# Optimization experiments

Measured on AMD Instinct MI355X. Metric: run time of the kernel, lower is better.

Reference implementation:

```python
import jax, jax.numpy as jnp
import numpy as np

B, TE, TD, EH, DH = 128, 512, 128, 512, 512
K_CNN, C_CNN = 7, 105

def setup_inputs() -> dict:
    key = jax.random.key(0)
    ks = jax.random.split(key, 20)
    n = lambda k, shp: jax.random.normal(k, shp, dtype=jnp.float32) * 0.05
    return {
        "LSTM": jax.random.normal(ks[0], (B, TE, EH), dtype=jnp.float32),
        "CNNs": jax.random.normal(ks[1], (B, K_CNN, C_CNN), dtype=jnp.float32),
        "Wa_w": n(ks[2], (TD, DH)), "Wa_b": n(ks[3], (TD,)),
        "Ua_w": n(ks[4], (TE, EH)), "Ua_b": n(ks[5], (TE,)),
        "va_w": n(ks[6], (1, TE + TD)), "va_b": n(ks[7], (1,)),
        "phi_w": n(ks[8], (EH, TE)), "phi_b": n(ks[9], (EH,)),
        "Wih": n(ks[10], (4 * DH, C_CNN + EH)), "Whh": n(ks[11], (4 * DH, DH)),
        "bih": n(ks[12], (4 * DH,)), "bhh": n(ks[13], (4 * DH,)),
        "wij_w": n(ks[14], (K_CNN, DH + C_CNN)), "wij_b": n(ks[15], (K_CNN,)),
        "s_i": jax.random.uniform(ks[16], (B, DH), dtype=jnp.float32),
        "m_i": jax.random.uniform(ks[17], (B, DH), dtype=jnp.float32),
    }

def reference(LSTM, CNNs, Wa_w, Wa_b, Ua_w, Ua_b, va_w, va_b, phi_w, phi_b,
              Wih, Whh, bih, bhh, wij_w, wij_b, s_i, m_i):
    Bn, Te, Eh = LSTM.shape
    Td = Wa_w.shape[0]
    Dh = s_i.shape[1]
    # delta_i_j for all j: strict lower-triangular one-hots [Te, Te]
    Dm = jnp.tril(jnp.ones((Te, Te), LSTM.dtype), k=-1)
    phi = Dm @ phi_w.T + phi_b                     # [Te, Eh]
    ph = phi[None, :, :] * LSTM                    # [B, Te, Eh] phi_delta * LSTM[:, j]
    Ua = jnp.einsum('bte,se->bts', ph, Ua_w) + Ua_b  # [B, Te, Te]
    Wa = s_i @ Wa_w.T + Wa_b                       # [B, Td] (same for all i, j)
    cat = jnp.concatenate([jnp.broadcast_to(Wa[:, None, :], (Bn, Te, Td)), Ua], axis=-1)
    Cw = jnp.tanh(cat) * va_w[0]                   # [B, Te, Td+Te]
    # one-hot mask picks index i + Te - j; v_a reduces to a single gathered term + bias
    idx = jnp.arange(Td)[:, None] + Te - jnp.arange(Te)[None, :]   # [Td, Te]
    e = Cw[:, jnp.arange(Te)[None, :], idx] + va_b[0]              # [B, Td, Te]
    a = jax.nn.softmax(e, axis=-1)
    c_i = jnp.einsum('bit,bte->bie', a, LSTM)      # [B, Td, Eh]
    # CNN attention (same for all decoder steps; note non-standard normalizer kept faithfully)
    w_cnn, w_s = wij_w[:, :C_CNN], wij_w[:, C_CNN:]
    ep = jnp.tanh(jnp.einsum('bkc,kc->bk', CNNs, w_cnn) + s_i @ w_s.T + wij_b)  # [B, K]
    ap = jnp.exp(ep) / jnp.sum(ep)
    c_p = jnp.einsum('bk,bkc->bc', ap, CNNs)       # [B, C_CNN]
    # LSTMCell with fixed (s_i, m_i) state => all decoder steps vectorize over i
    x = jnp.concatenate([c_i, jnp.broadcast_to(c_p[:, None, :], (Bn, Td, C_CNN))], axis=-1)
    gates = jnp.einsum('bid,gd->big', x, Wih) + bih + (s_i @ Whh.T + bhh)[:, None, :]
    ig, fg, gg, og = jnp.split(gates, 4, axis=-1)
    cnew = jax.nn.sigmoid(fg) * m_i[:, None, :] + jax.nn.sigmoid(ig) * jnp.tanh(gg)
    h = jax.nn.sigmoid(og) * jnp.tanh(cnew)        # [B, Td, Dh]
    return h
```

## Files before the change

kernel.cpp:

```cpp
#include <hip/hip_runtime.h>
#include <hip/hip_bf16.h>

#define B_   128
#define TE_  512
#define TD_  128
#define EH_  512
#define DH_  512
#define KC_  7
#define CC_  105
#define G_   2048
#define KX_  617
#define KP_  640
#define GNT  10

typedef __attribute__((ext_vector_type(8))) short bf16x8;
typedef __attribute__((ext_vector_type(4))) float f32x4;

__device__ __forceinline__ float sigm(float x){ return 1.f/(1.f + __expf(-x)); }
__device__ __forceinline__ float tanhf_fast(float x){
  float e = __expf(2.f*x);
  return 1.f - 2.f/(e + 1.f);
}

__device__ __forceinline__ unsigned short f2bf(float f){
  unsigned int u = __float_as_uint(f);
  unsigned int r = (u + 0x7fffu + ((u >> 16) & 1u)) >> 16;
  return (unsigned short)r;
}

typedef __attribute__((address_space(3))) unsigned int lds_u32_t;
typedef __attribute__((address_space(1))) const unsigned int glb_u32_t;
__device__ __forceinline__ void gload16(const void* g, void* l) {
  __builtin_amdgcn_global_load_lds((glb_u32_t*)g, (lds_u32_t*)l, 16, 0, 0);
}

static const size_t OFF_PHI  = 0;
static const size_t OFF_WA   = OFF_PHI  + (size_t)TE_*EH_*4;
static const size_t OFF_HPRE = OFF_WA   + (size_t)B_*TD_*4;
static const size_t OFF_EP   = OFF_HPRE + (size_t)B_*G_*4;
static const size_t OFF_CP   = OFF_EP   + 4096;
static const size_t OFF_ET   = ((OFF_CP + (size_t)B_*CC_*4 + 255)/256)*256;
static const size_t OFF_STAT = OFF_ET + (size_t)B_*TE_*TD_*4;
static const size_t OFF_P    = ((OFF_STAT + (size_t)2*B_*TD_*4 + 255)/256)*256;
static const size_t OFF_LT   = OFF_P  + (size_t)B_*TD_*TE_*2;
static const size_t OFF_WR   = OFF_LT + (size_t)B_*TE_*EH_*2;
static const size_t OFF_PT   = OFF_P;
static const size_t OFF_SUM  = OFF_PT + (size_t)TE_*EH_*4;
static const size_t OFF_WT   = OFF_P + (size_t)2*1024*1024;
static const size_t OFF_WAT  = OFF_P + (size_t)6*1024*1024;

__global__ __launch_bounds__(256) void k_tr(const float* __restrict__ src,
                                            float* __restrict__ dst, int R, int C) {
  int r0 = blockIdx.x * 64, c0 = blockIdx.y * 64;
  __shared__ float tile[64][65];
  int tid = threadIdx.x;
  int r = tid >> 2, c16 = (tid & 3) * 16;
  const float4* s4 = (const float4*)(src + (size_t)(r0 + r)*C + c0 + c16);
  float4 v0 = s4[0], v1 = s4[1], v2 = s4[2], v3 = s4[3];
  *(float4*)&tile[r][c16]    = v0;
  *(float4*)&tile[r][c16+4]  = v1;
  *(float4*)&tile[r][c16+8]  = v2;
  *(float4*)&tile[r][c16+12] = v3;
  __syncthreads();
  float o[16];
  #pragma unroll
  for (int j = 0; j < 16; ++j) o[j] = tile[c16+j][r];
  float* d = dst + (size_t)(c0 + r)*R + r0 + c16;
  *(float4*)d      = *(float4*)&o[0];
  *(float4*)(d+4)  = *(float4*)&o[4];
  *(float4*)(d+8)  = *(float4*)&o[8];
  *(float4*)(d+12) = *(float4*)&o[12];
}

__global__ void k_phiA(const float* __restrict__ phiT, float* __restrict__ phi,
                       float* __restrict__ sums) {
  int e = blockIdx.x * 256 + threadIdx.x;
  int z = blockIdx.y;
  float acc = 0.f;
  for (int t = z*64; t < z*64 + 64; ++t) {
    phi[(size_t)t*EH_ + e] = acc;
    acc += phiT[(size_t)t*EH_ + e];
  }
  sums[z*EH_ + e] = acc;
}
__global__ void k_phiB(const float* __restrict__ sums, const float* __restrict__ phi_b,
                       float* __restrict__ phi) {
  int e = blockIdx.x * 256 + threadIdx.x;
  int z = blockIdx.y;
  float off = phi_b[e];
  for (int zz = 0; zz < z; ++zz) off += sums[zz*EH_ + e];
  for (int t = z*64; t < z*64 + 64; ++t)
    phi[(size_t)t*EH_ + e] += off;
}

__global__ __launch_bounds__(256) void k_wa2(const float* __restrict__ s_i,
                                             const float* __restrict__ WaT,
                                             const float* __restrict__ Wa_b,
                                             const float* __restrict__ va_w,
                                             float* __restrict__ wa) {
  int lane = threadIdx.x & 63, wv = threadIdx.x >> 6;
  int b = blockIdx.x * 4 + wv;
  int d0 = lane * 2;
  const float2* w = (const float2*)WaT + lane;
  const float* s = s_i + (size_t)b*DH_;
  float ax = 0.f, ay = 0.f;
  #pragma unroll 8
  for (int k = 0; k < DH_; ++k) {
    float2 wv2 = w[(size_t)k*64];
    float x = s[k];
    ax += wv2.x * x; ay += wv2.y * x;
  }
  wa[b*TD_ + d0]     = tanhf_fast(ax + Wa_b[d0])     * va_w[d0];
  wa[b*TD_ + d0 + 1] = tanhf_fast(ay + Wa_b[d0 + 1]) * va_w[d0 + 1];
}

__global__ __launch_bounds__(64) void k_hpre2(const float* __restrict__ s_i,
                                              const float* __restrict__ WhhT,
                                              const float* __restrict__ bih,
                                              const float* __restrict__ bhh,
                                              float* __restrict__ hpre) {
  int gq = blockIdx.x * 64 + threadIdx.x;
  int b0 = blockIdx.y * 2;
  const float4* w = (const float4*)WhhT + gq;
  const float* s0 = s_i + (size_t)b0*DH_;
  const float* s1 = s0 + DH_;
  float4 a0 = {0.f,0.f,0.f,0.f}, a1 = {0.f,0.f,0.f,0.f};
  #pragma unroll 8
  for (int k = 0; k < DH_; ++k) {
    float4 wv = w[(size_t)k*512];
    float x0 = s0[k], x1 = s1[k];
    a0.x += wv.x*x0; a0.y += wv.y*x0; a0.z += wv.z*x0; a0.w += wv.w*x0;
    a1.x += wv.x*x1; a1.y += wv.y*x1; a1.z += wv.z*x1; a1.w += wv.w*x1;
  }
  int g = gq * 4;
  float4 bi = *(const float4*)(bih + g);
  float4 bh = *(const float4*)(bhh + g);
  float4 o0, o1;
  o0.x = a0.x + bi.x + bh.x; o0.y = a0.y + bi.y + bh.y;
  o0.z = a0.z + bi.z + bh.z; o0.w = a0.w + bi.w + bh.w;
  o1.x = a1.x + bi.x + bh.x; o1.y = a1.y + bi.y + bh.y;
  o1.z = a1.z + bi.z + bh.z; o1.w = a1.w + bi.w + bh.w;
  *(float4*)(hpre + (size_t)b0*G_ + g)       = o0;
  *(float4*)(hpre + (size_t)(b0+1)*G_ + g)   = o1;
}

__global__ __launch_bounds__(256) void k_ep(const float* __restrict__ CNNs,
                                            const float* __restrict__ wij_w,
                                            const float* __restrict__ wij_b,
                                            const float* __restrict__ s_i,
                                            float* __restrict__ ep) {
  int gw = blockIdx.x * 4 + (threadIdx.x >> 6);
  int lane = threadIdx.x & 63;
  if (gw >= B_*KC_) return;
  int b = gw / KC_, k = gw % KC_;
  const float* cr = CNNs + (size_t)(b*KC_ + k)*CC_;
  const float* wr = wij_w + (size_t)k*KX_;
  float acc = 0.f;
  for (int c = lane; c < CC_; c += 64) acc += cr[c] * wr[c];
  const float* sr = s_i + (size_t)b*DH_;
  const float* wsr = wr + CC_;
  #pragma unroll
  for (int j = 0; j < 8; ++j) { int h = lane + j*64; acc += sr[h] * wsr[h]; }
  #pragma unroll
  for (int m = 32; m; m >>= 1) acc += __shfl_xor(acc, m, 64);
  if (lane == 0) ep[gw] = tanhf_fast(acc + wij_b[k]);
}

__global__ void k_cnn_fin(const float* __restrict__ ep, const float* __restrict__ CNNs,
                          float* __restrict__ cp) {
  __shared__ float red[1024];
  __shared__ float apl[B_*KC_];
  int tid = threadIdx.x;
  red[tid] = (tid < B_*KC_) ? ep[tid] : 0.f;
  __syncthreads();
  for (int off = 512; off > 0; off >>= 1) {
    if (tid < off) red[tid] += red[tid + off];
    __syncthreads();
  }
  float S = red[0];
  if (tid < B_*KC_) apl[tid] = __expf(ep[tid]) / S;
  __syncthreads();
  for (int idx = tid; idx < B_*CC_; idx += blockDim.x) {
    int b = idx / CC_, c = idx % CC_;
    float acc = 0.f;
    #pragma unroll
    for (int k = 0; k < KC_; ++k)
      acc += apl[b*KC_ + k] * CNNs[(size_t)(b*KC_ + k)*CC_ + c];
    cp[idx] = acc;
  }
}

__global__ void k_cvtW(const float* __restrict__ Wih, unsigned short* __restrict__ Wr) {
  int id = blockIdx.x * 256 + threadIdx.x;
  int nr = id / 80, c8 = (id % 80) * 8;
  int gate = nr & 3, dh = nr >> 2;
  const float* src = Wih + (size_t)(gate*DH_ + dh)*KX_;
  unsigned short o[8];
  #pragma unroll
  for (int j = 0; j < 8; ++j) {
    int col = c8 + j;
    o[j] = (col < KX_) ? f2bf(src[col]) : 0;
  }
  *(uint4*)(Wr + (size_t)nr*KP_ + c8) = *(uint4*)o;
}

__global__ __launch_bounds__(256) void k_ltrans(const float* __restrict__ LSTM,
                                                unsigned short* __restrict__ LT) {
  int e0 = blockIdx.x * 64, t0 = blockIdx.y * 64, b = blockIdx.z;
  __shared__ float tile[64][65];
  int tid = threadIdx.x;
  int tt = tid >> 2, c16 = (tid & 3) * 16;
  const float4* src = (const float4*)(LSTM + ((size_t)b*TE_ + t0 + tt)*EH_ + e0 + c16);
  float4 v0 = src[0], v1 = src[1], v2 = src[2], v3 = src[3];
  *(float4*)&tile[tt][c16]    = v0;
  *(float4*)&tile[tt][c16+4]  = v1;
  *(float4*)&tile[tt][c16+8]  = v2;
  *(float4*)&tile[tt][c16+12] = v3;
  __syncthreads();
  int e = tid >> 2, t16 = (tid & 3) * 16;
  unsigned short o[16];
  #pragma unroll
  for (int j = 0; j < 16; ++j) o[j] = f2bf(tile[t16+j][e]);
  unsigned short* dst = LT + ((size_t)b*EH_ + e0 + e)*TE_ + t0 + t16;
  *(uint4*)dst     = *(uint4*)&o[0];
  *(uint4*)(dst+8) = *(uint4*)&o[8];
}

#define BMM_M 64
#define LDA_  40
#define LDB_  40
#define OTS_  132
__global__ __launch_bounds__(256) void k_bandmm(const float* __restrict__ LSTM,
                                                const float* __restrict__ phi,
                                                const float* __restrict__ Ua_w,
                                                const float* __restrict__ Ua_b,
                                                const float* __restrict__ va_w,
                                                const float* __restrict__ va_b,
                                                const float* __restrict__ wa,
                                                float* __restrict__ ET) {
  int t0 = blockIdx.x * BMM_M;
  int b  = blockIdx.y;
  int s_base = 321 - t0;
  __shared__ __align__(16) char smem[BMM_M * OTS_ * 4];
  short* sA = (short*)smem;
  short* sB = (short*)(smem + BMM_M*LDA_*2);
  int tid = threadIdx.x;
  int wave = tid >> 6, lane = tid & 63;
  int quad = lane >> 4, l16 = lane & 15;

  f32x4 acc[4][3];
  #pragma unroll
  for (int m = 0; m < 4; ++m)
    #pragma unroll
    for (int n = 0; n < 3; ++n)
      acc[m][n] = (f32x4){0.f, 0.f, 0.f, 0.f};

  int arow = tid >> 2;
  int ach  = (tid & 3) * 8;
  int aq   = ach >> 2;

  const float4* baseL = (const float4*)(LSTM + ((size_t)b*TE_ + t0 + arow)*EH_);
  const float4* baseP = (const float4*)(phi + (size_t)(t0 + arow)*EH_);
  const float4* baseU[3];
  int brow[3], bch[3];
  #pragma unroll
  for (int c = 0; c < 3; ++c) {
    int idx = c*256 + tid;
    brow[c] = idx >> 2;
    bch[c]  = (idx & 3) * 8;
    int s = s_base + brow[c];
    int sc = s < 0 ? 0 : (s > 511 ? 511 : s);
    baseU[c] = (const float4*)(Ua_w + (size_t)sc*EH_ + bch[c]);
  }

  float4 l0 = baseL[aq], l1 = baseL[aq+1], p0 = baseP[aq], p1 = baseP[aq+1];
  float4 u0[3], u1[3];
  #pragma unroll
  for (int c = 0; c < 3; ++c) { u0[c] = baseU[c][0]; u1[c] = baseU[c][1]; }

  for (int k0 = 0; k0 < EH_; k0 += 32) {
    unsigned short at[8];
    at[0]=f2bf(l0.x*p0.x); at[1]=f2bf(l0.y*p0.y); at[2]=f2bf(l0.z*p0.z); at[3]=f2bf(l0.w*p0.w);
    at[4]=f2bf(l1.x*p1.x); at[5]=f2bf(l1.y*p1.y); at[6]=f2bf(l1.z*p1.z); at[7]=f2bf(l1.w*p1.w);
    unsigned short bt[3][8];
    #pragma unroll
    for (int c = 0; c < 3; ++c) {
      bt[c][0]=f2bf(u0[c].x); bt[c][1]=f2bf(u0[c].y); bt[c][2]=f2bf(u0[c].z); bt[c][3]=f2bf(u0[c].w);
      bt[c][4]=f2bf(u1[c].x); bt[c][5]=f2bf(u1[c].y); bt[c][6]=f2bf(u1[c].z); bt[c][7]=f2bf(u1[c].w);
    }
    if (k0 + 32 < EH_) {
      int q = (k0 + 32) >> 2;
      l0 = baseL[q+aq]; l1 = baseL[q+aq+1]; p0 = baseP[q+aq]; p1 = baseP[q+aq+1];
      #pragma unroll
      for (int c = 0; c < 3; ++c) { u0[c] = baseU[c][q]; u1[c] = baseU[c][q+1]; }
    }
    __syncthreads();
    *(uint4*)&sA[arow*LDA_ + ach] = *(uint4*)at;
    #pragma unroll
    for (int c = 0; c < 3; ++c)
      *(uint4*)&sB[brow[c]*LDB_ + bch[c]] = *(uint4*)bt[c];
    __syncthreads();
    bf16x8 bfr[3];
    #pragma unroll
    for (int n = 0; n < 3; ++n)
      bfr[n] = *(const bf16x8*)&sB[(l16 + (wave*3 + n)*16)*LDB_ + quad*8];
    #pragma unroll
    for (int m = 0; m < 4; ++m) {
      bf16x8 af = *(const bf16x8*)&sA[(l16 + m*16)*LDA_ + quad*8];
      #pragma unroll
      for (int n = 0; n < 3; ++n)
        acc[m][n] = __builtin_amdgcn_mfma_f32_16x16x32_bf16(af, bfr[n], acc[m][n], 0, 0, 0);
    }
  }

  __syncthreads();
  float* tileO = (float*)smem;
  float vb = va_b[0];
  #pragma unroll
  for (int n = 0; n < 3; ++n) {
    int s = s_base + wave*48 + n*16 + l16;
    float ub = (s >= 0 && s < TE_) ? Ua_b[s] : 0.f;
    float vw = (s >= 0 && s < TE_) ? va_w[TD_ + s] : 0.f;
    #pragma unroll
    for (int m = 0; m < 4; ++m) {
      #pragma unroll
      for (int r = 0; r < 4; ++r) {
        int tl = m*16 + quad*4 + r;
        int i = s + t0 + tl - 384;
        if (i >= 0 && i < TD_) {
          float val;
          if (s >= 0) val = tanhf_fast(acc[m][n][r] + ub) * vw + vb;
          else        val = wa[b*TD_ + s + 128] + vb;
          tileO[tl*OTS_ + i] = val;
        }
      }
    }
  }
  __syncthreads();
  {
    int rsub = tid >> 5, c4 = (tid & 31) * 4;
    #pragma unroll
    for (int p = 0; p < 8; ++p) {
      int row = p*8 + rsub;
      float4 v = *(const float4*)&tileO[row*OTS_ + c4];
      *(float4*)(ET + ((size_t)b*TE_ + t0 + row)*TD_ + c4) = v;
    }
  }
}

__global__ __launch_bounds__(256) void k_stats(const float* __restrict__ ET,
                                               float* __restrict__ stat) {
  int i0 = blockIdx.x * 64, b = blockIdx.y;
  __shared__ float red[4][64], smax[64];
  int tid = threadIdx.x;
  int q = tid >> 6, il = tid & 63;
  const float* col = ET + (size_t)b*TE_*TD_ + i0 + il;
  float m = -1e30f;
  for (int t = q*128; t < q*128 + 128; ++t) m = fmaxf(m, col[(size_t)t*TD_]);
  red[q][il] = m;
  __syncthreads();
  if (tid < 64) {
    float mm = fmaxf(fmaxf(red[0][tid], red[1][tid]), fmaxf(red[2][tid], red[3][tid]));
    smax[tid] = mm;
  }
  __syncthreads();
  float mm = smax[il];
  float s = 0.f;
  for (int t = q*128; t < q*128 + 128; ++t) s += __expf(col[(size_t)t*TD_] - mm);
  __syncthreads();
  red[q][il] = s;
  __syncthreads();
  if (tid < 64) {
    float ss = red[0][tid] + red[1][tid] + red[2][tid] + red[3][tid];
    stat[b*TD_ + i0 + tid] = smax[tid];
    stat[(size_t)B_*TD_ + b*TD_ + i0 + tid] = 1.f/ss;
  }
}

__global__ __launch_bounds__(256) void k_trP(const float* __restrict__ ET,
                                             const float* __restrict__ stat,
                                             unsigned short* __restrict__ P) {
  int t0 = blockIdx.x * 64, i0 = blockIdx.y * 64, b = blockIdx.z;
  __shared__ float tile[64][65];
  __shared__ float smL[64], svL[64];
  int tid = threadIdx.x;
  if (tid < 64) {
    smL[tid] = stat[b*TD_ + i0 + tid];
    svL[tid] = stat[(size_t)B_*TD_ + b*TD_ + i0 + tid];
  }
  int tt = tid >> 2, c16 = (tid & 3) * 16;
  const float4* src = (const float4*)(ET + ((size_t)b*TE_ + t0 + tt)*TD_ + i0 + c16);
  float4 v[4]; v[0] = src[0]; v[1] = src[1]; v[2] = src[2]; v[3] = src[3];
  __syncthreads();
  const float* vf = (const float*)v;
  #pragma unroll
  for (int j = 0; j < 16; ++j)
    tile[tt][c16+j] = __expf(vf[j] - smL[c16+j]) * svL[c16+j];
  __syncthreads();
  int i = tid >> 2, t16 = (tid & 3) * 16;
  unsigned short o[16];
  #pragma unroll
  for (int j = 0; j < 16; ++j) o[j] = f2bf(tile[t16+j][i]);
  unsigned short* dst = P + ((size_t)b*TD_ + i0 + i)*TE_ + t0 + t16;
  *(uint4*)dst     = *(uint4*)&o[0];
  *(uint4*)(dst+8) = *(uint4*)&o[8];
}

__global__ void k_cp_fill(const float* __restrict__ cp, unsigned short* __restrict__ X) {
  int id = blockIdx.x * 256 + threadIdx.x;
  int m = id >> 4, c8 = (id & 15) * 8;
  int b = m >> 7;
  unsigned short o[8];
  #pragma unroll
  for (int j = 0; j < 8; ++j) {
    int c = c8 + j;
    o[j] = (c < CC_) ? f2bf(cp[b*CC_ + c]) : 0;
  }
  *(uint4*)(X + (size_t)m*KP_ + EH_ + c8) = *(uint4*)o;
}

#define CI_LD 40
__global__ __launch_bounds__(256) void k_ci_mm(const unsigned short* __restrict__ P,
                                               const unsigned short* __restrict__ LT,
                                               unsigned short* __restrict__ X) {
  int b = blockIdx.x, e0 = blockIdx.y * 128;
  __shared__ short sA[128 * CI_LD];
  __shared__ short sB[128 * CI_LD];
  int tid = threadIdx.x;
  int wave = tid >> 6, lane = tid & 63, quad = lane >> 4, l16 = lane & 15;
  int wm = wave >> 1, wn = wave & 1;
  int row = tid >> 1, ho = (tid & 1) * 16;

  const unsigned short* pa = P + ((size_t)b*TD_ + row)*TE_ + ho;
  const unsigned short* pb = LT + ((size_t)b*EH_ + e0 + row)*TE_ + ho;

  f32x4 acc[4][4];
  #pragma unroll
  for (int m = 0; m < 4; ++m)
    #pragma unroll
    for (int n = 0; n < 4; ++n)
      acc[m][n] = (f32x4){0.f, 0.f, 0.f, 0.f};

  uint4 a0 = *(const uint4*)pa, a1 = *(const uint4*)(pa + 8);
  uint4 b0 = *(const uint4*)pb, b1 = *(const uint4*)(pb + 8);

  for (int k0 = 0; k0 < TE_; k0 += 32) {
    uint4 na0, na1, nb0, nb1;
    if (k0 + 32 < TE_) {
      na0 = *(const uint4*)(pa + k0 + 32); na1 = *(const uint4*)(pa + k0 + 40);
      nb0 = *(const uint4*)(pb + k0 + 32); nb1 = *(const uint4*)(pb + k0 + 40);
    }
    __syncthreads();
    *(uint4*)&sA[row*CI_LD + ho]     = a0;
    *(uint4*)&sA[row*CI_LD + ho + 8] = a1;
    *(uint4*)&sB[row*CI_LD + ho]     = b0;
    *(uint4*)&sB[row*CI_LD + ho + 8] = b1;
    __syncthreads();
    bf16x8 bfr[4];
    #pragma unroll
    for (int n = 0; n < 4; ++n)
      bfr[n] = *(const bf16x8*)&sB[(wn*64 + n*16 + l16)*CI_LD + quad*8];
    #pragma unroll
    for (int m = 0; m < 4; ++m) {
      bf16x8 af = *(const bf16x8*)&sA[(wm*64 + m*16 + l16)*CI_LD + quad*8];
      #pragma unroll
      for (int n = 0; n < 4; ++n)
        acc[m][n] = __builtin_amdgcn_mfma_f32_16x16x32_bf16(af, bfr[n], acc[m][n], 0, 0, 0);
    }
    a0 = na0; a1 = na1; b0 = nb0; b1 = nb1;
  }

  #pragma unroll
  for (int m = 0; m < 4; ++m) {
    int i = wm*64 + m*16 + quad*4;
    #pragma unroll
    for (int n = 0; n < 4; ++n) {
      int e = e0 + wn*64 + n*16 + l16;
      unsigned short* xp = X + ((size_t)b*TD_ + i)*KP_ + e;
      #pragma unroll
      for (int r = 0; r < 4; ++r)
        xp[(size_t)r*KP_] = f2bf(acc[m][n][r]);
    }
  }
}

__global__ __launch_bounds__(512, 2) void k_gates8(const unsigned short* __restrict__ Wr,
                                                   const unsigned short* __restrict__ X,
                                                   const float* __restrict__ hpre,
                                                   const float* __restrict__ m_i,
                                                   float* __restrict__ out) {
  __shared__ short lds[4 * 256 * 64];
  const int g0  = blockIdx.x * 256;
  const int mi0 = blockIdx.y * 256;
  const int tid  = threadIdx.x;
  const int wave = tid >> 6, lane = tid & 63;
  const int l16 = lane & 15, quad = lane >> 4;
  const int wr = wave >> 2, wc = wave & 3;

  const int srow8 = lane >> 3;
  const int sch   = (lane & 7) ^ srow8;
  const unsigned short* gA = Wr + (size_t)(g0  + wave*8 + srow8) * KP_ + sch*8;
  const unsigned short* gB = X  + (size_t)(mi0 + wave*8 + srow8) * KP_ + sch*8;
  short* lA0 = lds;
  short* lB0 = lds + 16384;
  short* lA1 = lds + 32768;
  short* lB1 = lds + 49152;

  f32x4 acc[8][4];
  #pragma unroll
  for (int m = 0; m < 8; ++m)
    #pragma unroll
    for (int n = 0; n < 4; ++n) acc[m][n] = (f32x4){0.f, 0.f, 0.f, 0.f};

  auto stage = [&](int kt, int bf) {
    short* la = bf ? lA1 : lA0;
    short* lb = bf ? lB1 : lB0;
    const unsigned short* ga = gA + kt*64;
    const unsigned short* gb = gB + kt*64;
    #pragma unroll
    for (int r = 0; r < 4; ++r) {
      gload16(ga + (size_t)r*64*KP_, la + (r*8 + wave)*512);
      gload16(gb + (size_t)r*64*KP_, lb + (r*8 + wave)*512);
    }
  };

  stage(0, 0);
  __syncthreads();

  const int x7 = l16 & 7;
  for (int kt = 0; kt < GNT; ++kt) {
    const int cur = kt & 1;
    if (kt + 1 < GNT) stage(kt + 1, cur ^ 1);
    const short* la = cur ? lA1 : lA0;
    const short* lb = cur ? lB1 : lB0;
    #pragma unroll
    for (int ks = 0; ks < 2; ++ks) {
      const int ck = ((((ks << 2) | quad) ^ x7) << 3);
      bf16x8 bv[4];
      #pragma unroll
      for (int n = 0; n < 4; ++n)
        bv[n] = *(const bf16x8*)&lb[(wc*64 + n*16 + l16)*64 + ck];
      #pragma unroll
      for (int qm = 0; qm < 2; ++qm) {
        bf16x8 av[4];
        #pragma unroll
        for (int m = 0; m < 4; ++m)
          av[m] = *(const bf16x8*)&la[(wr*128 + qm*64 + m*16 + l16)*64 + ck];
        __builtin_amdgcn_s_setprio(1);
        #pragma unroll
        for (int m = 0; m < 4; ++m)
          #pragma unroll
          for (int n = 0; n < 4; ++n)
            acc[qm*4 + m][n] = __builtin_amdgcn_mfma_f32_16x16x32_bf16(av[m], bv[n], acc[qm*4 + m][n], 0, 0, 0);
        __builtin_amdgcn_s_setprio(0);
      }
    }
    __syncthreads();
  }

  const int bb = (mi0 >> 7) + (wc >> 1);
  const float* hp = hpre + (size_t)bb * G_;
  #pragma unroll
  for (int M = 0; M < 8; ++M) {
    const int dh = (g0 >> 2) + wr*32 + M*4 + quad;
    float h0 = hp[dh], h1 = hp[DH_ + dh], h2 = hp[2*DH_ + dh], h3 = hp[3*DH_ + dh];
    float miv = m_i[(size_t)bb*DH_ + dh];
    #pragma unroll
    for (int n = 0; n < 4; ++n) {
      int mi = mi0 + wc*64 + n*16 + l16;
      float ig = acc[M][n][0] + h0;
      float fg = acc[M][n][1] + h1;
      float gg = acc[M][n][2] + h2;
      float og = acc[M][n][3] + h3;
      float c  = sigm(fg)*miv + sigm(ig)*tanhf_fast(gg);
      float h  = sigm(og)*tanhf_fast(c);
      out[(size_t)mi*DH_ + dh] = h;
    }
  }
}

extern "C" void kernel_launch(void* const* d_in, const int* in_sizes, int n_in,
                              void* d_out, int out_size, void* d_ws, size_t ws_size,
                              hipStream_t stream) {
  (void)in_sizes; (void)n_in; (void)out_size; (void)ws_size;
  const float* LSTM  = (const float*)d_in[0];
  const float* CNNs  = (const float*)d_in[1];
  const float* Wa_w  = (const float*)d_in[2];
  const float* Wa_b  = (const float*)d_in[3];
  const float* Ua_w  = (const float*)d_in[4];
  const float* Ua_b  = (const float*)d_in[5];
  const float* va_w  = (const float*)d_in[6];
  const float* va_b  = (const float*)d_in[7];
  const float* phi_w = (const float*)d_in[8];
  const float* phi_b = (const float*)d_in[9];
  const float* Wih   = (const float*)d_in[10];
  const float* Whh   = (const float*)d_in[11];
  const float* bih   = (const float*)d_in[12];
  const float* bhh   = (const float*)d_in[13];
  const float* wij_w = (const float*)d_in[14];
  const float* wij_b = (const float*)d_in[15];
  const float* s_i   = (const float*)d_in[16];
  const float* m_i   = (const float*)d_in[17];
  float* out = (float*)d_out;
  char* ws = (char*)d_ws;

  float* phi  = (float*)(ws + OFF_PHI);
  float* wa   = (float*)(ws + OFF_WA);
  float* hpre = (float*)(ws + OFF_HPRE);
  float* ep   = (float*)(ws + OFF_EP);
  float* cp   = (float*)(ws + OFF_CP);
  float* stat = (float*)(ws + OFF_STAT);
  float* ET   = (float*)(ws + OFF_ET);
  unsigned short* X  = (unsigned short*)(ws + OFF_ET);
  unsigned short* P  = (unsigned short*)(ws + OFF_P);
  unsigned short* LT = (unsigned short*)(ws + OFF_LT);
  unsigned short* Wr = (unsigned short*)(ws + OFF_WR);
  float* phiT        = (float*)(ws + OFF_PT);
  float* sums        = (float*)(ws + OFF_SUM);
  float* WhhT        = (float*)(ws + OFF_WT);
  float* WaT         = (float*)(ws + OFF_WAT);

  k_tr      <<<dim3(8,8),      dim3(256),  0, stream>>>(phi_w, phiT, 512, 512);
  k_tr      <<<dim3(32,8),     dim3(256),  0, stream>>>(Whh, WhhT, 2048, 512);
  k_tr      <<<dim3(2,8),      dim3(256),  0, stream>>>(Wa_w, WaT, 128, 512);
  k_phiA    <<<dim3(2,8),      dim3(256),  0, stream>>>(phiT, phi, sums);
  k_phiB    <<<dim3(2,8),      dim3(256),  0, stream>>>(sums, phi_b, phi);
  k_wa2     <<<dim3(32),       dim3(256),  0, stream>>>(s_i, WaT, Wa_b, va_w, wa);
  k_hpre2   <<<dim3(8,64),     dim3(64),   0, stream>>>(s_i, WhhT, bih, bhh, hpre);
  k_ep      <<<dim3(224),      dim3(256),  0, stream>>>(CNNs, wij_w, wij_b, s_i, ep);
  k_cnn_fin <<<dim3(1),        dim3(1024), 0, stream>>>(ep, CNNs, cp);
  k_cvtW    <<<dim3(640),      dim3(256),  0, stream>>>(Wih, Wr);
  k_ltrans  <<<dim3(8,8,128),  dim3(256),  0, stream>>>(LSTM, LT);
  k_bandmm  <<<dim3(8,128),    dim3(256),  0, stream>>>(LSTM, phi, Ua_w, Ua_b, va_w, va_b, wa, ET);
  k_stats   <<<dim3(2,128),    dim3(256),  0, stream>>>(ET, stat);
  k_trP     <<<dim3(8,2,128),  dim3(256),  0, stream>>>(ET, stat, P);
  k_cp_fill <<<dim3(1024),     dim3(256),  0, stream>>>(cp, X);
  k_ci_mm   <<<dim3(128,4),    dim3(256),  0, stream>>>(P, LT, X);
  k_gates8  <<<dim3(8,64),     dim3(512),  0, stream>>>(Wr, X, hpre, m_i, out);
}
```

Before: 532.6 us.

## Fuse softmax stats and transpose into one LDS-tiled kernel; fuse CNN context fill

Measured after the change: 489.0 us. 8.2% less time.

```diff
diff --git a/kernel.cpp b/kernel.cpp
--- a/kernel.cpp
+++ b/kernel.cpp
@@ -114,34 +114,29 @@
   wa[b*TD_ + d0 + 1] = tanhf_fast(ay + Wa_b[d0 + 1]) * va_w[d0 + 1];
 }
 
-__global__ __launch_bounds__(64) void k_hpre2(const float* __restrict__ s_i,
-                                              const float* __restrict__ WhhT,
-                                              const float* __restrict__ bih,
-                                              const float* __restrict__ bhh,
-                                              float* __restrict__ hpre) {
-  int gq = blockIdx.x * 64 + threadIdx.x;
-  int b0 = blockIdx.y * 2;
+__global__ __launch_bounds__(256) void k_hpre2(const float* __restrict__ s_i,
+                                               const float* __restrict__ WhhT,
+                                               const float* __restrict__ bih,
+                                               const float* __restrict__ bhh,
+                                               float* __restrict__ hpre) {
+  int gq = blockIdx.x * 256 + threadIdx.x;
+  int b  = blockIdx.y;
   const float4* w = (const float4*)WhhT + gq;
-  const float* s0 = s_i + (size_t)b0*DH_;
-  const float* s1 = s0 + DH_;
-  float4 a0 = {0.f,0.f,0.f,0.f}, a1 = {0.f,0.f,0.f,0.f};
+  const float* s = s_i + (size_t)b*DH_;
+  float4 a = {0.f,0.f,0.f,0.f};
   #pragma unroll 8
   for (int k = 0; k < DH_; ++k) {
     float4 wv = w[(size_t)k*512];
-    float x0 = s0[k], x1 = s1[k];
-    a0.x += wv.x*x0; a0.y += wv.y*x0; a0.z += wv.z*x0; a0.w += wv.w*x0;
-    a1.x += wv.x*x1; a1.y += wv.y*x1; a1.z += wv.z*x1; a1.w += wv.w*x1;
+    float x = s[k];
+    a.x += wv.x*x; a.y += wv.y*x; a.z += wv.z*x; a.w += wv.w*x;
   }
   int g = gq * 4;
   float4 bi = *(const float4*)(bih + g);
   float4 bh = *(const float4*)(bhh + g);
-  float4 o0, o1;
-  o0.x = a0.x + bi.x + bh.x; o0.y = a0.y + bi.y + bh.y;
-  o0.z = a0.z + bi.z + bh.z; o0.w = a0.w + bi.w + bh.w;
-  o1.x = a1.x + bi.x + bh.x; o1.y = a1.y + bi.y + bh.y;
-  o1.z = a1.z + bi.z + bh.z; o1.w = a1.w + bi.w + bh.w;
-  *(float4*)(hpre + (size_t)b0*G_ + g)       = o0;
-  *(float4*)(hpre + (size_t)(b0+1)*G_ + g)   = o1;
+  float4 o;
+  o.x = a.x + bi.x + bh.x; o.y = a.y + bi.y + bh.y;
+  o.z = a.z + bi.z + bh.z; o.w = a.w + bi.w + bh.w;
+  *(float4*)(hpre + (size_t)b*G_ + g) = o;
 }
 
 __global__ __launch_bounds__(256) void k_ep(const float* __restrict__ CNNs,
@@ -166,10 +161,8 @@
   if (lane == 0) ep[gw] = tanhf_fast(acc + wij_b[k]);
 }
 
-__global__ void k_cnn_fin(const float* __restrict__ ep, const float* __restrict__ CNNs,
-                          float* __restrict__ cp) {
+__global__ void k_epsum(const float* __restrict__ ep, float* __restrict__ epsum) {
   __shared__ float red[1024];
-  __shared__ float apl[B_*KC_];
   int tid = threadIdx.x;
   red[tid] = (tid < B_*KC_) ? ep[tid] : 0.f;
   __syncthreads();
@@ -177,17 +170,28 @@
     if (tid < off) red[tid] += red[tid + off];
     __syncthreads();
   }
-  float S = red[0];
-  if (tid < B_*KC_) apl[tid] = __expf(ep[tid]) / S;
-  __syncthreads();
-  for (int idx = tid; idx < B_*CC_; idx += blockDim.x) {
-    int b = idx / CC_, c = idx % CC_;
-    float acc = 0.f;
+  if (tid == 0) epsum[0] = red[0];
+}
+
+__global__ __launch_bounds__(128) void k_cp(const float* __restrict__ ep,
+                                            const float* __restrict__ epsum,
+                                            const float* __restrict__ CNNs,
+                                            unsigned short* __restrict__ X) {
+  int b = blockIdx.x, c = threadIdx.x;
+  float S = epsum[0];
+  float apl[KC_];
+  #pragma unroll
+  for (int k = 0; k < KC_; ++k) apl[k] = __expf(ep[b*KC_ + k]) / S;
+  float acc = 0.f;
+  if (c < CC_) {
     #pragma unroll
     for (int k = 0; k < KC_; ++k)
-      acc += apl[b*KC_ + k] * CNNs[(size_t)(b*KC_ + k)*CC_ + c];
-    cp[idx] = acc;
-  }
+      acc += apl[k] * CNNs[(size_t)(b*KC_ + k)*CC_ + c];
+  }
+  unsigned short o = (c < CC_) ? f2bf(acc) : 0;
+  unsigned short* xb = X + (size_t)b*TD_*KP_ + EH_ + c;
+  for (int i = 0; i < TD_; ++i)
+    xb[(size_t)i*KP_] = o;
 }
 
 __global__ void k_cvtW(const float* __restrict__ Wih, unsigned short* __restrict__ Wr) {
@@ -348,75 +352,77 @@
   }
 }
 
-__global__ __launch_bounds__(256) void k_stats(const float* __restrict__ ET,
-                                               float* __restrict__ stat) {
+#define SMX_LD 65
+__global__ __launch_bounds__(512) void k_smx(const float* __restrict__ ET,
+                                             unsigned short* __restrict__ P) {
   int i0 = blockIdx.x * 64, b = blockIdx.y;
-  __shared__ float red[4][64], smax[64];
+  __shared__ float tile[TE_][SMX_LD];
+  __shared__ float red[8][64], smax[64], sinv[64];
   int tid = threadIdx.x;
-  int q = tid >> 6, il = tid & 63;
-  const float* col = ET + (size_t)b*TE_*TD_ + i0 + il;
-  float m = -1e30f;
-  for (int t = q*128; t < q*128 + 128; ++t) m = fmaxf(m, col[(size_t)t*TD_]);
-  red[q][il] = m;
+
+  {
+    int r = tid >> 2, c16 = (tid & 3) * 16;
+    #pragma unroll
+    for (int rep = 0; rep < 4; ++rep) {
+      int t = rep*128 + r;
+      const float4* s4 = (const float4*)(ET + ((size_t)b*TE_ + t)*TD_ + i0 + c16);
+      float4 v0 = s4[0], v1 = s4[1], v2 = s4[2], v3 = s4[3];
+      *(float4*)&tile[t][c16]    = v0;
+      *(float4*)&tile[t][c16+4]  = v1;
+      *(float4*)&tile[t][c16+8]  = v2;
+      *(float4*)&tile[t][c16+12] = v3;
+    }
+  }
+  __syncthreads();
+
+  int i = tid & 63, seg = tid >> 6;
+  {
+    float m = -1e30f;
+    for (int t = seg*64; t < seg*64 + 64; ++t) m = fmaxf(m, tile[t][i]);
+    red[seg][i] = m;
+  }
   __syncthreads();
   if (tid < 64) {
-    float mm = fmaxf(fmaxf(red[0][tid], red[1][tid]), fmaxf(red[2][tid], red[3][tid]));
-    smax[tid] = mm;
-  }
-  __syncthreads();
-  float mm = smax[il];
-  float s = 0.f;
-  for (int t = q*128; t < q*128 + 128; ++t) s += __expf(col[(size_t)t*TD_] - mm);
-  __syncthreads();
-  red[q][il] = s;
+    float m = red[0][tid];
+    #pragma unroll
+    for (int s = 1; s < 8; ++s) m = fmaxf(m, red[s][tid]);
+    smax[tid] = m;
+  }
+  __syncthreads();
+  {
+    float mm = smax[i];
+    float s = 0.f;
+    for (int t = seg*64; t < seg*64 + 64; ++t) {
+      float v = __expf(tile[t][i] - mm);
+      tile[t][i] = v;
+      s += v;
+    }
+    red[seg][i] = s;
+  }
   __syncthreads();
   if (tid < 64) {
-    float ss = red[0][tid] + red[1][tid] + red[2][tid] + red[3][tid];
-    stat[b*TD_ + i0 + tid] = smax[tid];
-    stat[(size_t)B_*TD_ + b*TD_ + i0 + tid] = 1.f/ss;
-  }
-}
-
-__global__ __launch_bounds__(256) void k_trP(const float* __restrict__ ET,
-                                             const float* __restrict__ stat,
-                                             unsigned short* __restrict__ P) {
-  int t0 = blockIdx.x * 64, i0 = blockIdx.y * 64, b = blockIdx.z;
-  __shared__ float tile[64][65];
-  __shared__ float smL[64], svL[64];
-  int tid = threadIdx.x;
-  if (tid < 64) {
-    smL[tid] = stat[b*TD_ + i0 + tid];
-    svL[tid] = stat[(size_t)B_*TD_ + b*TD_ + i0 + tid];
-  }
-  int tt = tid >> 2, c16 = (tid & 3) * 16;
-  const float4* src = (const float4*)(ET + ((size_t)b*TE_ + t0 + tt)*TD_ + i0 + c16);
-  float4 v[4]; v[0] = src[0]; v[1] = src[1]; v[2] = src[2]; v[3] = src[3];
-  __syncthreads();
-  const float* vf = (const float*)v;
-  #pragma unroll
-  for (int j = 0; j < 16; ++j)
-    tile[tt][c16+j] = __expf(vf[j] - smL[c16+j]) * svL[c16+j];
-  __syncthreads();
-  int i = tid >> 2, t16 = (tid & 3) * 16;
-  unsigned short o[16];
-  #pragma unroll
-  for (int j = 0; j < 16; ++j) o[j] = f2bf(tile[t16+j][i]);
-  unsigned short* dst = P + ((size_t)b*TD_ + i0 + i)*TE_ + t0 + t16;
-  *(uint4*)dst     = *(uint4*)&o[0];
-  *(uint4*)(dst+8) = *(uint4*)&o[8];
-}
-
-__global__ void k_cp_fill(const float* __restrict__ cp, unsigned short* __restrict__ X) {
-  int id = blockIdx.x * 256 + threadIdx.x;
-  int m = id >> 4, c8 = (id & 15) * 8;
-  int b = m >> 7;
-  unsigned short o[8];
-  #pragma unroll
-  for (int j = 0; j < 8; ++j) {
-    int c = c8 + j;
-    o[j] = (c < CC_) ? f2bf(cp[b*CC_ + c]) : 0;
-  }
-  *(uint4*)(X + (size_t)m*KP_ + EH_ + c8) = *(uint4*)o;
+    float s = red[0][tid];
+    #pragma unroll
+    for (int sg = 1; sg < 8; ++sg) s += red[sg][tid];
+    sinv[tid] = 1.f / s;
+  }
+  __syncthreads();
+  {
+    int tidq = tid & 255, half = tid >> 8;
+    int ii = tidq >> 2, t16 = (tidq & 3) * 16;
+    float inv = sinv[ii];
+    #pragma unroll
+    for (int tt = 0; tt < 4; ++tt) {
+      int tb = (tt*2 + half) * 64;
+      unsigned short o[16];
+      #pragma unroll
+      for (int j = 0; j < 16; ++j)
+        o[j] = f2bf(tile[tb + t16 + j][ii] * inv);
+      unsigned short* dst = P + ((size_t)b*TD_ + i0 + ii)*TE_ + tb + t16;
+      *(uint4*)dst     = *(uint4*)&o[0];
+      *(uint4*)(dst+8) = *(uint4*)&o[8];
+    }
+  }
 }
 
 #define CI_LD 40
@@ -608,8 +614,7 @@
   float* wa   = (float*)(ws + OFF_WA);
   float* hpre = (float*)(ws + OFF_HPRE);
   float* ep   = (float*)(ws + OFF_EP);
-  float* cp   = (float*)(ws + OFF_CP);
-  float* stat = (float*)(ws + OFF_STAT);
+  float* epsum= (float*)(ws + OFF_EP) + 1000;
   float* ET   = (float*)(ws + OFF_ET);
   unsigned short* X  = (unsigned short*)(ws + OFF_ET);
   unsigned short* P  = (unsigned short*)(ws + OFF_P);
@@ -626,15 +631,14 @@
   k_phiA    <<<dim3(2,8),      dim3(256),  0, stream>>>(phiT, phi, sums);
   k_phiB    <<<dim3(2,8),      dim3(256),  0, stream>>>(sums, phi_b, phi);
   k_wa2     <<<dim3(32),       dim3(256),  0, stream>>>(s_i, WaT, Wa_b, va_w, wa);
-  k_hpre2   <<<dim3(8,64),     dim3(64),   0, stream>>>(s_i, WhhT, bih, bhh, hpre);
+  k_hpre2   <<<dim3(2,128),    dim3(256),  0, stream>>>(s_i, WhhT, bih, bhh, hpre);
   k_ep      <<<dim3(224),      dim3(256),  0, stream>>>(CNNs, wij_w, wij_b, s_i, ep);
-  k_cnn_fin <<<dim3(1),        dim3(1024), 0, stream>>>(ep, CNNs, cp);
+  k_epsum   <<<dim3(1),        dim3(1024), 0, stream>>>(ep, epsum);
   k_cvtW    <<<dim3(640),      dim3(256),  0, stream>>>(Wih, Wr);
   k_ltrans  <<<dim3(8,8,128),  dim3(256),  0, stream>>>(LSTM, LT);
   k_bandmm  <<<dim3(8,128),    dim3(256),  0, stream>>>(LSTM, phi, Ua_w, Ua_b, va_w, va_b, wa, ET);
-  k_stats   <<<dim3(2,128),    dim3(256),  0, stream>>>(ET, stat);
-  k_trP     <<<dim3(8,2,128),  dim3(256),  0, stream>>>(ET, stat, P);
-  k_cp_fill <<<dim3(1024),     dim3(256),  0, stream>>>(cp, X);
+  k_smx     <<<dim3(2,128),    dim3(512),  0, stream>>>(ET, P);
+  k_cp      <<<dim3(128),      dim3(128),  0, stream>>>(ep, epsum, CNNs, X);
   k_ci_mm   <<<dim3(128,4),    dim3(256),  0, stream>>>(P, LT, X);
   k_gates8  <<<dim3(8,64),     dim3(512),  0, stream>>>(Wr, X, hpre, m_i, out);
 }
```
